# Optimization experiments

Measured on AMD Instinct MI355X. Metric: run time of the kernel, lower is better.

The kernel has to match this reference:

```python
import jax, jax.numpy as jnp
import numpy as np

N_NODES = 100000
N_EDGES = 1600000
N_GRAPHS = 512
N_REL = 4
N_TYPES = 13
EMB = 128
HID = 128
BN_EPS = 1e-5
L2_EPS = 1e-12


def setup_inputs() -> dict:
    key = jax.random.key(0)
    ks = jax.random.split(key, 16)
    node_type = jax.random.randint(ks[0], (N_NODES,), 0, N_TYPES)
    x = jax.nn.one_hot(node_type, N_TYPES, dtype=jnp.float32)  # [N,13] one-hot
    edge_index = jax.random.randint(ks[1], (2, N_EDGES), 0, N_NODES)
    edge_type = jax.random.randint(ks[2], (N_EDGES,), 0, N_REL)
    batch = jnp.sort(jax.random.randint(ks[3], (N_NODES,), 0, N_GRAPHS))
    s = 0.05
    return {
        "x": x,
        "edge_index": edge_index,
        "edge_type": edge_type,
        "batch": batch,
        "emb": jax.random.normal(ks[4], (N_TYPES, EMB), jnp.float32) * s,
        "Wrel": jax.random.normal(ks[5], (2, N_REL, HID, HID), jnp.float32) * s,  # layer0 in=EMB==HID
        "Wroot": jax.random.normal(ks[6], (2, HID, HID), jnp.float32) * s,
        "conv_bias": jnp.zeros((2, HID), jnp.float32),
        "bn_gamma": jnp.ones((2, HID), jnp.float32),
        "bn_beta": jnp.zeros((2, HID), jnp.float32),
        "prelu_a": jnp.full((2,), 0.25, jnp.float32),
        "fc1_w": jax.random.normal(ks[7], (HID, 256), jnp.float32) * s,
        "fc1_b": jnp.zeros((256,), jnp.float32),
        "fc2_w": jax.random.normal(ks[8], (256, 128), jnp.float32) * s,
        "fc2_b": jnp.zeros((128,), jnp.float32),
        "out_w": jax.random.normal(ks[9], (128, 1), jnp.float32) * s,
        "out_b": jnp.zeros((1,), jnp.float32),
    }


def _rgcn_conv(h, Wrel, Wroot, bias, src, dst, edge_type):
    # PyG RGCNConv: out = h @ Wroot + bias + sum_r mean_{edges of rel r}(h_src @ W_r)
    n = h.shape[0]
    out = h @ Wroot + bias
    for r in range(N_REL):
        m = (edge_type == r).astype(h.dtype)  # [E]
        hr = h @ Wrel[r]                       # [N, dout]
        msg = hr[src] * m[:, None]             # gather + mask  [E, dout]
        num = jax.ops.segment_sum(msg, dst, num_segments=n)
        cnt = jax.ops.segment_sum(m, dst, num_segments=n)
        out = out + num / jnp.maximum(cnt, 1.0)[:, None]
    return out


def _batchnorm(h, gamma, beta):
    mu = jnp.mean(h, axis=0)
    var = jnp.mean((h - mu) ** 2, axis=0)  # biased var (training-mode BN)
    return (h - mu) * jax.lax.rsqrt(var + BN_EPS) * gamma + beta


def reference(x, edge_index, edge_type, batch, emb, Wrel, Wroot, conv_bias,
              bn_gamma, bn_beta, prelu_a, fc1_w, fc1_b, fc2_w, fc2_b, out_w, out_b):
    src, dst = edge_index[0], edge_index[1]
    idx = jnp.argmax(x, axis=1)         # torch.nonzero(one_hot)[1]
    h = emb[idx]                        # [N, EMB]
    for l in range(2):
        h = _rgcn_conv(h, Wrel[l], Wroot[l], conv_bias[l], src, dst, edge_type)
        h = _batchnorm(h, bn_gamma[l], bn_beta[l])
        h = jnp.where(h >= 0, h, prelu_a[l] * h)  # PReLU
        nrm = jnp.sqrt(jnp.sum(h * h, axis=1, keepdims=True))
        h = h / jnp.maximum(nrm, L2_EPS)          # F.normalize(p=2, dim=1)
    # global mean pool over graphs
    pooled = jax.ops.segment_sum(h, batch, num_segments=N_GRAPHS)
    cnt = jax.ops.segment_sum(jnp.ones((h.shape[0],), h.dtype), batch, num_segments=N_GRAPHS)
    g = pooled / jnp.maximum(cnt, 1.0)[:, None]   # [G, HID]
    g = jax.nn.relu(g @ fc1_w + fc1_b)
    g = jax.nn.relu(g @ fc2_w + fc2_b)
    return g @ out_w + out_b                      # [G, 1]
```

## Files before the change

kernel.cpp:

```cpp
#include <hip/hip_runtime.h>
#include <hip/hip_bf16.h>

#define NN 100000
#define NE 1600000
#define NG 512
#define CH3 65536
#define CHW 16384
#define NCH 2
#define BPC 128
#define ES 12500


typedef __attribute__((ext_vector_type(8))) short short8;
typedef __attribute__((ext_vector_type(4))) float float4v;


__device__ inline int lower_bound_dev(const int* __restrict__ a, int n, int v) {
    int lo = 0, hi = n;
    while (lo < hi) { int mid = (lo + hi) >> 1; if (a[mid] < v) lo = mid + 1; else hi = mid; }
    return lo;
}

__device__ inline unsigned short f2bf(float x) {
    unsigned u = __float_as_uint(x);
    unsigned r = (u + 0x7fffu + ((u >> 16) & 1u)) >> 16;
    return (unsigned short)r;
}

__device__ inline float bf2f(unsigned short h) {
    return __uint_as_float((unsigned)h << 16);
}


__global__ void node_type_kernel(const float* __restrict__ x, int* __restrict__ idx, int n) {
    int i = blockIdx.x * blockDim.x + threadIdx.x;
    if (i >= n) return;
    const float* row = x + (size_t)i * 13;
    int b = 0;
    #pragma unroll
    for (int t = 0; t < 13; ++t) if (row[t] > 0.5f) { b = t; }
    idx[i] = b;
}


__global__ void build_weights(const float* __restrict__ emb, const float* __restrict__ Wroot,
                              const float* __restrict__ Wrel,
                              unsigned short* __restrict__ Bf, unsigned short* __restrict__ B0f,
                              float* __restrict__ bnSums) {
    if (blockIdx.x < 8) bnSums[blockIdx.x * 256 + threadIdx.x] = 0.f;
    int i = blockIdx.x * 256 + threadIdx.x;
    if (i < 81920) {
        int j = i & 7;
        int lane = (i >> 3) & 63;
        int t = (i >> 9) & 7;
        int ks = (i >> 12) & 3;
        int kc = i >> 14;
        int n = t * 16 + (lane & 15);
        int kcol = j * 16 + ks * 4 + (lane >> 4);
        float w;
        if (kc == 0) w = Wroot[16384 + (size_t)kcol * 128 + n];
        else {
            int r = kc - 1;
            w = Wrel[(((size_t)(4 + r) * 128) + kcol) * 128 + n];
        }
        Bf[i] = f2bf(w);
    } else {
        int i0 = i - 81920;
        int j = i0 & 7;
        int lane = (i0 >> 3) & 63;
        int t = (i0 >> 9) & 7;
        int ks = i0 >> 12;
        int n = t * 16 + (lane & 15);
        int p = ks * 32 + (lane >> 4) * 8 + j;
        float val = 0.f;
        if (p < 32) {
            if (p < 13) {
                const float* er = emb + (size_t)p * 128;
                const float* wc = Wroot + n;
                float acc = 0.f;
                for (int k = 0; k < 128; ++k) acc += er[k] * wc[(size_t)k * 128];
                val = acc;
            }
        } else {
            int r = (p - 32) >> 4, tt = (p - 32) & 15;
            if (tt < 13) {
                const float* er = emb + (size_t)tt * 128;
                const float* wc = Wrel + ((size_t)r * 128) * 128 + n;
                float acc = 0.f;
                for (int k = 0; k < 128; ++k) acc += er[k] * wc[(size_t)k * 128];
                val = acc;
            }
        }
        B0f[i0] = f2bf(val);
    }
}


__global__ __launch_bounds__(256) void hist_kernel(const int* __restrict__ dst,
                                                   const int* __restrict__ src,
                                                   const int* __restrict__ et,
                                                   const int* __restrict__ ntype,
                                                   int* __restrict__ srcT,
                                                   unsigned* __restrict__ partials) {
    __shared__ unsigned h[CHW];
    const int b = blockIdx.x, c = blockIdx.y;
    const int lo = c * CH3;
    for (int i = threadIdx.x; i < CHW; i += 256) h[i] = 0;
    __syncthreads();
    const int e0 = b * ES;
    const int e1 = (e0 + ES < NE) ? e0 + ES : NE;
    if (c == 0) {
        for (int e = e0 + threadIdx.x; e < e1; e += 256) {
            int k = dst[e] - lo;
            if (k >= 0 && k < CH3) atomicAdd(&h[k >> 2], 1u << ((k & 3) << 3));
            int s = src[e];
            srcT[e] = s | (ntype[s] << 17) | (et[e] << 21);
        }
    } else {
        for (int e = e0 + threadIdx.x; e < e1; e += 256) {
            int k = dst[e] - lo;
            if (k >= 0 && k < CH3) atomicAdd(&h[k >> 2], 1u << ((k & 3) << 3));
        }
    }
    __syncthreads();
    unsigned* out = partials + ((size_t)(c * BPC + b)) * CHW;
    for (int i = threadIdx.x; i < CHW; i += 256) out[i] = h[i];
}

__global__ void hist_reduce(unsigned* __restrict__ partials, int* __restrict__ counts) {
    const int c = blockIdx.y;
    const int i = blockIdx.x * 256 + threadIdx.x;
    size_t base = (size_t)c * BPC * CHW + i;
    unsigned r0 = 0, r1 = 0, r2 = 0, r3 = 0;
    #pragma unroll 4
    for (int b = 0; b < BPC; ++b) {
        unsigned t = partials[base + (size_t)b * CHW];
        partials[base + (size_t)b * CHW] = r0 | (r1 << 8) | (r2 << 16) | (r3 << 24);
        r0 += t & 0xffu; r1 += (t >> 8) & 0xffu; r2 += (t >> 16) & 0xffu; r3 += t >> 24;
    }
    int k0 = c * CH3 + 4 * i;
    if (k0 < NN)     counts[k0]     = (int)r0;
    if (k0 + 1 < NN) counts[k0 + 1] = (int)r1;
    if (k0 + 2 < NN) counts[k0 + 2] = (int)r2;
    if (k0 + 3 < NN) counts[k0 + 3] = (int)r3;
}

__global__ __launch_bounds__(256) void scan1(const int* __restrict__ counts, int* __restrict__ offs,
                                             int* __restrict__ bsums, int n) {
    __shared__ int wsum[4];
    const int base = blockIdx.x * 1024 + threadIdx.x * 4;
    int v[4]; int loc = 0;
    #pragma unroll
    for (int j = 0; j < 4; ++j) { int idx = base + j; v[j] = (idx < n) ? counts[idx] : 0; loc += v[j]; }
    const int lane = threadIdx.x & 63, wid = threadIdx.x >> 6;
    int sc = loc;
    #pragma unroll
    for (int o = 1; o < 64; o <<= 1) { int t = __shfl_up(sc, o, 64); if (lane >= o) sc += t; }
    if (lane == 63) wsum[wid] = sc;
    __syncthreads();
    int wbase = 0;
    for (int w = 0; w < wid; ++w) wbase += wsum[w];
    int run = wbase + sc - loc;
    #pragma unroll
    for (int j = 0; j < 4; ++j) { int idx = base + j; if (idx < n) offs[idx] = run; run += v[j]; }
    if (threadIdx.x == 255) bsums[blockIdx.x] = wbase + sc;
}

__global__ void scan2(int* __restrict__ bsums, int* __restrict__ offs, int nb, int n) {
    const int lane = threadIdx.x;
    int carry = 0;
    for (int base = 0; base < nb; base += 64) {
        int idx = base + lane;
        int v = (idx < nb) ? bsums[idx] : 0;
        int sc = v;
        #pragma unroll
        for (int o = 1; o < 64; o <<= 1) { int t = __shfl_up(sc, o, 64); if (lane >= o) sc += t; }
        if (idx < nb) bsums[idx] = carry + sc - v;
        int tot = __shfl(sc, 63, 64);
        carry += tot;
    }
    if (lane == 0) offs[n] = carry;
}

__global__ __launch_bounds__(256) void scan3(int* __restrict__ offs, const int* __restrict__ bsums, int n) {
    const int s = bsums[blockIdx.x];
    const int base = blockIdx.x * 1024 + threadIdx.x * 4;
    #pragma unroll
    for (int j = 0; j < 4; ++j) { int idx = base + j; if (idx < n) offs[idx] += s; }
}

__global__ __launch_bounds__(256) void place_kernel(const int* __restrict__ dst,
                                                    const int* __restrict__ srcT,
                                                    const int* __restrict__ offs,
                                                    const unsigned* __restrict__ partials,
                                                    int* __restrict__ sortedSrc) {
    __shared__ unsigned cur[CHW];
    const int b = blockIdx.x, c = blockIdx.y;
    const int lo = c * CH3;
    const unsigned* pb = partials + ((size_t)(c * BPC + b)) * CHW;
    for (int i = threadIdx.x; i < CHW; i += 256) cur[i] = pb[i];
    __syncthreads();
    const int e0 = b * ES;
    const int e1 = (e0 + ES < NE) ? e0 + ES : NE;
    for (int e = e0 + threadIdx.x; e < e1; e += 256) {
        int key = dst[e];
        int k = key - lo;
        if (k >= 0 && k < CH3) {
            int sh = (k & 3) << 3;
            unsigned old = atomicAdd(&cur[k >> 2], 1u << sh);
            int my = (int)((old >> sh) & 0xffu);
            int pos = offs[key] + my;
            sortedSrc[pos] = srcT[e];
        }
    }
}


__global__ __launch_bounds__(256) void gemm0_fused(const int* __restrict__ sortedSrc,
                                                   const int* __restrict__ offs,
                                                   const int* __restrict__ ntype,
                                                   const unsigned short* __restrict__ B0f,
                                                   const float* __restrict__ bias,
                                                   unsigned short* __restrict__ Cb,
                                                   float* __restrict__ bnSums, int M) {
    __shared__ unsigned short A0L[12 * 128 * 8];
    __shared__ unsigned cnt[128][13];
    __shared__ float sred[2][4][128];
    const int tid = threadIdx.x;

    if (tid < 128) {
        const int n = blockIdx.x * 128 + tid;
        const int tile = tid >> 4, l16 = tid & 15;
        if (n < M) {
            #pragma unroll
            for (int t = 0; t < 13; ++t) cnt[tid][t] = 0;
            const int o0 = offs[n], o1 = offs[n + 1];
            unsigned relc = 0;
            for (int i = o0; i < o1; ++i) {
                int v = sortedSrc[i];
                int ty = (v >> 17) & 15, r = v >> 21;
                cnt[tid][ty] += 1u << (r << 3);
                relc += 1u << (r << 3);
            }
            float inv[4];
            #pragma unroll
            for (int r = 0; r < 4; ++r) {
                unsigned c = (relc >> (r << 3)) & 0xffu;
                inv[r] = 1.0f / (float)(c > 0 ? c : 1);
            }
            const int myty = ntype[n];
            #pragma unroll
            for (int ks = 0; ks < 3; ++ks) {
                #pragma unroll
                for (int quad = 0; quad < 4; ++quad) {
                    unsigned short vals[8];
                    #pragma unroll
                    for (int j = 0; j < 8; ++j) {
                        int p = ks * 32 + quad * 8 + j;
                        float v;
                        if (p < 32) v = (p == myty) ? 1.0f : 0.0f;
                        else {
                            int r = (p - 32) >> 4, tt = (p - 32) & 15;
                            v = (tt < 13) ? (float)((cnt[tid][tt] >> (r << 3)) & 0xffu) * inv[r] : 0.0f;
                        }
                        vals[j] = f2bf(v);
                    }
                    const int C = ks * 4 + quad;
                    *(uint4*)(A0L + (C * 128 + tile * 16 + l16) * 8) = *(uint4*)vals;
                }
            }
        } else {
            uint4 z; z.x = 0; z.y = 0; z.z = 0; z.w = 0;
            #pragma unroll
            for (int C = 0; C < 12; ++C)
                *(uint4*)(A0L + (C * 128 + tile * 16 + l16) * 8) = z;
        }
    }
    __syncthreads();

    const int wv = tid >> 6, lane = tid & 63;
    const int l16 = lane & 15, quad = lane >> 4;
    const int rowbase = blockIdx.x * 128 + wv * 32;
    const int tileL0 = wv * 2, tileL1 = wv * 2 + 1;

    float4v acc[2][8];
    #pragma unroll
    for (int t = 0; t < 8; ++t) {
        float bv = bias[t * 16 + l16];
        float4v av = {bv, bv, bv, bv};
        acc[0][t] = av; acc[1][t] = av;
    }

    const unsigned short* bl = B0f + lane * 8;
    #pragma unroll
    for (int ks = 0; ks < 3; ++ks) {
        const int C = ks * 4 + quad;
        short8 af0 = *(const short8*)(A0L + (C * 128 + tileL0 * 16 + l16) * 8);
        short8 af1 = *(const short8*)(A0L + (C * 128 + tileL1 * 16 + l16) * 8);
        const unsigned short* bp = bl + ((ks * 8) << 9);
        #pragma unroll
        for (int t = 0; t < 8; ++t) {
            short8 bf = *(const short8*)(bp + (t << 9));
            acc[0][t] = __builtin_amdgcn_mfma_f32_16x16x32_bf16(af0, bf, acc[0][t], 0, 0, 0);
            acc[1][t] = __builtin_amdgcn_mfma_f32_16x16x32_bf16(af1, bf, acc[1][t], 0, 0, 0);
        }
    }

    #pragma unroll
    for (int h = 0; h < 2; ++h) {
        #pragma unroll
        for (int rg = 0; rg < 4; ++rg) {
            int rr = rowbase + h * 16 + quad * 4 + rg;
            if (rr < M) {
                unsigned short v[8];
                #pragma unroll
                for (int t = 0; t < 8; ++t) v[t] = f2bf(acc[h][t][rg]);
                *(uint4*)(Cb + (size_t)rr * 128 + l16 * 8) = *(uint4*)v;
            }
        }
    }
    float s[8], q[8];
    #pragma unroll
    for (int t = 0; t < 8; ++t) {
        s[t] = 0.f; q[t] = 0.f;
        #pragma unroll
        for (int h = 0; h < 2; ++h) {
            #pragma unroll
            for (int rg = 0; rg < 4; ++rg) {
                int rr = rowbase + h * 16 + quad * 4 + rg;
                if (rr < M) { float v = acc[h][t][rg]; s[t] += v; q[t] += v * v; }
            }
        }
    }
    #pragma unroll
    for (int t = 0; t < 8; ++t) {
        s[t] += __shfl_down(s[t], 32, 64); q[t] += __shfl_down(q[t], 32, 64);
        s[t] += __shfl_down(s[t], 16, 64); q[t] += __shfl_down(q[t], 16, 64);
    }
    if (lane < 16) {
        #pragma unroll
        for (int t = 0; t < 8; ++t) {
            sred[0][wv][t * 16 + l16] = s[t];
            sred[1][wv][t * 16 + l16] = q[t];
        }
    }
    __syncthreads();
    if (tid < 128) {
        float S = sred[0][0][tid] + sred[0][1][tid] + sred[0][2][tid] + sred[0][3][tid];
        float Q = sred[1][0][tid] + sred[1][1][tid] + sred[1][2][tid] + sred[1][3][tid];
        float* bnS = bnSums + ((blockIdx.x & 7) << 8);
        unsafeAtomicAdd(bnS + tid, S);
        unsafeAtomicAdd(bnS + 128 + tid, Q);
    }
}


__global__ __launch_bounds__(256) void gather_gemm1(const unsigned short* __restrict__ hbf,
                                                    const int* __restrict__ sortedSrc,
                                                    const int* __restrict__ offs,
                                                    const unsigned short* __restrict__ Bf,
                                                    const float* __restrict__ bias,
                                                    unsigned short* __restrict__ Cb,
                                                    float* __restrict__ bnSums) {
    __shared__ unsigned short rootL[2048];
    __shared__ unsigned short aggL[8192];
    const int tid = threadIdx.x;
    const int tile = blockIdx.x;
    {
        const int l16g = tid >> 4;
        const int cidx = tid & 15;
        const int c8 = cidx << 3;
        const int n = tile * 16 + l16g;
        const int pu = cidx * 16 + (l16g ^ cidx);
        uint4 ru = *(const uint4*)(hbf + (size_t)n * 128 + c8);
        *(uint4*)(rootL + pu * 8) = ru;

        const unsigned short* hb = hbf + c8;
        const int o0 = offs[n], o1 = offs[n + 1];

        float a0[8], a1[8], a2[8], a3[8];
        #pragma unroll
        for (int j = 0; j < 8; ++j) { a0[j] = 0.f; a1[j] = 0.f; a2[j] = 0.f; a3[j] = 0.f; }
        float c0 = 0.f, c1 = 0.f, c2 = 0.f, c3 = 0.f;

        auto body = [&](int v, uint4 u) {
            int r = v >> 21;
            float f[8];
            f[0] = __uint_as_float(u.x << 16); f[1] = __uint_as_float(u.x & 0xffff0000u);
            f[2] = __uint_as_float(u.y << 16); f[3] = __uint_as_float(u.y & 0xffff0000u);
            f[4] = __uint_as_float(u.z << 16); f[5] = __uint_as_float(u.z & 0xffff0000u);
            f[6] = __uint_as_float(u.w << 16); f[7] = __uint_as_float(u.w & 0xffff0000u);
            float m0 = (r == 0) ? 1.f : 0.f, m1 = (r == 1) ? 1.f : 0.f;
            float m2 = (r == 2) ? 1.f : 0.f, m3 = (r == 3) ? 1.f : 0.f;
            c0 += m0; c1 += m1; c2 += m2; c3 += m3;
            #pragma unroll
            for (int j = 0; j < 8; ++j) {
                a0[j] = fmaf(m0, f[j], a0[j]);
                a1[j] = fmaf(m1, f[j], a1[j]);
                a2[j] = fmaf(m2, f[j], a2[j]);
                a3[j] = fmaf(m3, f[j], a3[j]);
            }
        };

        int i = o0;
        for (; i + 4 <= o1; i += 4) {
            int v0 = sortedSrc[i], v1 = sortedSrc[i + 1];
            int v2 = sortedSrc[i + 2], v3 = sortedSrc[i + 3];
            uint4 u0 = *(const uint4*)(hb + (size_t)(v0 & 0x1ffff) * 128);
            uint4 u1 = *(const uint4*)(hb + (size_t)(v1 & 0x1ffff) * 128);
            uint4 u2 = *(const uint4*)(hb + (size_t)(v2 & 0x1ffff) * 128);
            uint4 u3 = *(const uint4*)(hb + (size_t)(v3 & 0x1ffff) * 128);
            body(v0, u0); body(v1, u1); body(v2, u2); body(v3, u3);
        }
        if (i + 2 <= o1) {
            int v0 = sortedSrc[i], v1 = sortedSrc[i + 1];
            uint4 u0 = *(const uint4*)(hb + (size_t)(v0 & 0x1ffff) * 128);
            uint4 u1 = *(const uint4*)(hb + (size_t)(v1 & 0x1ffff) * 128);
            body(v0, u0); body(v1, u1);
            i += 2;
        }
        if (i < o1) {
            int v0 = sortedSrc[i];
            uint4 u0 = *(const uint4*)(hb + (size_t)(v0 & 0x1ffff) * 128);
            body(v0, u0);
        }

        const float i0 = 1.f / fmaxf(c0, 1.f), i1 = 1.f / fmaxf(c1, 1.f);
        const float i2 = 1.f / fmaxf(c2, 1.f), i3 = 1.f / fmaxf(c3, 1.f);
        unsigned short* bp = aggL + pu * 8;
        auto pack = [&](float* a, float inv, unsigned short* dp) {
            unsigned short v[8];
            #pragma unroll
            for (int j = 0; j < 8; ++j) v[j] = f2bf(a[j] * inv);
            *(uint4*)dp = *(uint4*)v;
        };
        pack(a0, i0, bp);
        pack(a1, i1, bp + 2048);
        pack(a2, i2, bp + 4096);
        pack(a3, i3, bp + 6144);
    }
    __syncthreads();

    const int wv = tid >> 6, lane = tid & 63;
    const int l16 = lane & 15, quad = lane >> 4;
    const int t0 = wv << 1;
    float4v acc0, acc1;
    {
        float b0v = bias[t0 * 16 + l16];
        float b1v = bias[(t0 + 1) * 16 + l16];
        float4v a0v = {b0v, b0v, b0v, b0v};
        float4v a1v = {b1v, b1v, b1v, b1v};
        acc0 = a0v; acc1 = a1v;
    }
    const unsigned short* bl = Bf + lane * 8;
    #pragma unroll
    for (int kc = 0; kc < 5; ++kc) {
        const unsigned short* Abase = (kc == 0) ? rootL : (aggL + (kc - 1) * 2048);
        #pragma unroll
        for (int ks = 0; ks < 4; ++ks) {
            const int C = ks * 4 + quad;
            const int p = C * 16 + (l16 ^ C);
            short8 af = *(const short8*)(Abase + p * 8);
            const unsigned short* bp = bl + (((kc * 4 + ks) * 8 + t0) << 9);
            short8 b0 = *(const short8*)(bp);
            short8 b1 = *(const short8*)(bp + 512);
            acc0 = __builtin_amdgcn_mfma_f32_16x16x32_bf16(af, b0, acc0, 0, 0, 0);
            acc1 = __builtin_amdgcn_mfma_f32_16x16x32_bf16(af, b1, acc1, 0, 0, 0);
        }
    }
    const int rowbase = tile * 16;
    #pragma unroll
    for (int rg = 0; rg < 4; ++rg) {
        int rr = rowbase + quad * 4 + rg;
        unsigned pk = (unsigned)f2bf(acc0[rg]) | ((unsigned)f2bf(acc1[rg]) << 16);
        *(unsigned*)(Cb + (size_t)rr * 128 + l16 * 8 + t0) = pk;
    }
    float s0 = 0.f, q0 = 0.f, s1 = 0.f, q1 = 0.f;
    #pragma unroll
    for (int rg = 0; rg < 4; ++rg) {
        float v0 = acc0[rg], v1 = acc1[rg];
        s0 += v0; q0 += v0 * v0; s1 += v1; q1 += v1 * v1;
    }
    s0 += __shfl_down(s0, 32, 64); q0 += __shfl_down(q0, 32, 64);
    s1 += __shfl_down(s1, 32, 64); q1 += __shfl_down(q1, 32, 64);
    s0 += __shfl_down(s0, 16, 64); q0 += __shfl_down(q0, 16, 64);
    s1 += __shfl_down(s1, 16, 64); q1 += __shfl_down(q1, 16, 64);
    if (lane < 16) {
        float* bnS = bnSums + ((tile & 7) << 8);
        unsafeAtomicAdd(bnS + t0 * 16 + l16, s0);
        unsafeAtomicAdd(bnS + 128 + t0 * 16 + l16, q0);
        unsafeAtomicAdd(bnS + (t0 + 1) * 16 + l16, s1);
        unsafeAtomicAdd(bnS + 128 + (t0 + 1) * 16 + l16, q1);
    }
}


__global__ void bn_finalize0(float* __restrict__ bnSums, float* __restrict__ fin, int n) {
    const int c = threadIdx.x;
    if (c < 128) {
        float s = 0.f, q = 0.f;
        #pragma unroll
        for (int j = 0; j < 8; ++j) { s += bnSums[j * 256 + c]; q += bnSums[j * 256 + 128 + c]; }
        const float invn = 1.0f / (float)n;
        float mu = s * invn;
        float var = q * invn - mu * mu; if (var < 0.f) var = 0.f;
        fin[c] = mu;
        fin[128 + c] = rsqrtf(var + 1e-5f);
    }
    __syncthreads();
    for (int i = c; i < 2048; i += 256) bnSums[i] = 0.f;
}


__global__ void bn_finalize(const float* __restrict__ bnSums, float* __restrict__ fin,
                            float* __restrict__ g0zero, int n) {
    const int c = threadIdx.x;
    if (g0zero) g0zero[blockIdx.x * 128 + c] = 0.f;
    if (blockIdx.x != 0) return;
    float s = 0.f, q = 0.f;
    #pragma unroll
    for (int j = 0; j < 8; ++j) { s += bnSums[j * 256 + c]; q += bnSums[j * 256 + 128 + c]; }
    const float invn = 1.0f / (float)n;
    float mu = s * invn;
    float var = q * invn - mu * mu; if (var < 0.f) var = 0.f;
    fin[c] = mu;
    fin[128 + c] = rsqrtf(var + 1e-5f);
}


__global__ __launch_bounds__(256) void bn_apply_kernel(const unsigned short* __restrict__ Cb,
                                unsigned short* __restrict__ hbf,
                                const float* __restrict__ fin,
                                const float* __restrict__ gamma, const float* __restrict__ beta,
                                const float* __restrict__ prelu_a, int layer) {
    const int tid = threadIdx.x;
    const int row = blockIdx.x * 16 + (tid >> 4);
    const int li = tid & 15;
    const int p8 = li << 3;
    const float a = prelu_a[layer];
    uint4 u = *(const uint4*)(Cb + (size_t)row * 128 + p8);
    float v[8];
    v[0] = __uint_as_float(u.x << 16); v[1] = __uint_as_float(u.x & 0xffff0000u);
    v[2] = __uint_as_float(u.y << 16); v[3] = __uint_as_float(u.y & 0xffff0000u);
    v[4] = __uint_as_float(u.z << 16); v[5] = __uint_as_float(u.z & 0xffff0000u);
    v[6] = __uint_as_float(u.w << 16); v[7] = __uint_as_float(u.w & 0xffff0000u);
    float t[8]; float ss = 0.f;
    #pragma unroll
    for (int j = 0; j < 8; ++j) {
        int cc = j * 16 + li;
        float tv = (v[j] - fin[cc]) * fin[128 + cc] * gamma[cc] + beta[cc];
        tv = (tv >= 0.f) ? tv : a * tv;
        t[j] = tv; ss += tv * tv;
    }
    ss += __shfl_xor(ss, 1, 64);
    ss += __shfl_xor(ss, 2, 64);
    ss += __shfl_xor(ss, 4, 64);
    ss += __shfl_xor(ss, 8, 64);
    const float scale = 1.0f / fmaxf(sqrtf(ss), 1e-12f);
    unsigned short o[8];
    #pragma unroll
    for (int j = 0; j < 8; ++j) o[j] = f2bf(t[j] * scale);
    *(uint4*)(hbf + (size_t)row * 128 + p8) = *(uint4*)o;
}


__global__ __launch_bounds__(256) void bn_apply_pool(const unsigned short* __restrict__ Cb,
                                const float* __restrict__ fin,
                                const float* __restrict__ gamma, const float* __restrict__ beta,
                                const float* __restrict__ prelu_a,
                                const int* __restrict__ batch,
                                float* __restrict__ g0) {
    __shared__ float P[16][128];
    __shared__ int gids[16];
    const int tid = threadIdx.x;
    const int r16 = tid >> 4;
    const int li = tid & 15;
    const int row = blockIdx.x * 16 + r16;
    const int p8 = li << 3;
    if (li == 0) gids[r16] = batch[row];
    const float a = prelu_a[1];
    uint4 u = *(const uint4*)(Cb + (size_t)row * 128 + p8);
    float v[8];
    v[0] = __uint_as_float(u.x << 16); v[1] = __uint_as_float(u.x & 0xffff0000u);
    v[2] = __uint_as_float(u.y << 16); v[3] = __uint_as_float(u.y & 0xffff0000u);
    v[4] = __uint_as_float(u.z << 16); v[5] = __uint_as_float(u.z & 0xffff0000u);
    v[6] = __uint_as_float(u.w << 16); v[7] = __uint_as_float(u.w & 0xffff0000u);
    float t[8]; float ss = 0.f;
    #pragma unroll
    for (int j = 0; j < 8; ++j) {
        int cc = j * 16 + li;
        float tv = (v[j] - fin[cc]) * fin[128 + cc] * gamma[cc] + beta[cc];
        tv = (tv >= 0.f) ? tv : a * tv;
        t[j] = tv; ss += tv * tv;
    }
    ss += __shfl_xor(ss, 1, 64);
    ss += __shfl_xor(ss, 2, 64);
    ss += __shfl_xor(ss, 4, 64);
    ss += __shfl_xor(ss, 8, 64);
    const float scale = 1.0f / fmaxf(sqrtf(ss), 1e-12f);
    #pragma unroll
    for (int j = 0; j < 8; ++j) P[r16][p8 + j] = t[j] * scale;
    __syncthreads();
    if (tid < 128) {
        int cur = gids[0];
        float run = 0.f;
        #pragma unroll
        for (int rr = 0; rr < 16; ++rr) {
            int g = gids[rr];
            if (g != cur) {
                unsafeAtomicAdd(&g0[(size_t)cur * 128 + tid], run);
                run = 0.f; cur = g;
            }
            run += P[rr][tid];
        }
        unsafeAtomicAdd(&g0[(size_t)cur * 128 + tid], run);
    }
}


__global__ void fc1_kernel(const float* __restrict__ g, const float* __restrict__ w,
                           const float* __restrict__ b, const int* __restrict__ batch,
                           float* __restrict__ o) {
    const int row = blockIdx.x;
    const int j = threadIdx.x;
    const int lo = lower_bound_dev(batch, NN, row);
    const int hi = lower_bound_dev(batch, NN, row + 1);
    const int c = hi - lo;
    const float invc = 1.0f / (float)(c > 0 ? c : 1);
    float acc = 0.f;
    #pragma unroll 8
    for (int k = 0; k < 128; ++k) {
        int lk = (k & 7) * 16 + (k >> 3);
        acc += g[row * 128 + k] * w[lk * 256 + j];
    }
    o[row * 256 + j] = fmaxf(acc * invc + b[j], 0.f);
}

__global__ void fc2_kernel(const float* __restrict__ g, const float* __restrict__ w,
                           const float* __restrict__ b, float* __restrict__ o) {
    const int row = blockIdx.x;
    const int j = threadIdx.x;
    float acc = b[j];
    #pragma unroll 8
    for (int k = 0; k < 256; ++k) acc += g[row * 256 + k] * w[k * 128 + j];
    o[row * 128 + j] = fmaxf(acc, 0.f);
}

__global__ void fco_kernel(const float* __restrict__ g, const float* __restrict__ w,
                           const float* __restrict__ b, float* __restrict__ o) {
    const int row = blockIdx.x * blockDim.x + threadIdx.x;
    if (row >= NG) return;
    float acc = b[0];
    #pragma unroll 8
    for (int k = 0; k < 128; ++k) acc += g[row * 128 + k] * w[k];
    o[row] = acc;
}


extern "C" void kernel_launch(void* const* d_in, const int* in_sizes, int n_in,
                              void* d_out, int out_size, void* d_ws, size_t ws_size,
                              hipStream_t stream) {
    const float* x      = (const float*)d_in[0];
    const int*   eidx   = (const int*)d_in[1];
    const int*   etype  = (const int*)d_in[2];
    const int*   batch  = (const int*)d_in[3];
    const float* emb    = (const float*)d_in[4];
    const float* Wrel   = (const float*)d_in[5];
    const float* Wroot  = (const float*)d_in[6];
    const float* cbias  = (const float*)d_in[7];
    const float* gamma  = (const float*)d_in[8];
    const float* beta   = (const float*)d_in[9];
    const float* prelua = (const float*)d_in[10];
    const float* fc1w   = (const float*)d_in[11];
    const float* fc1b   = (const float*)d_in[12];
    const float* fc2w   = (const float*)d_in[13];
    const float* fc2b   = (const float*)d_in[14];
    const float* outw   = (const float*)d_in[15];
    const float* outb   = (const float*)d_in[16];
    float* out = (float*)d_out;

    const int* src = eidx;
    const int* dst = eidx + NE;

    char* p = (char*)d_ws;
    auto alloc = [&](size_t bytes) { char* r = p; p += (bytes + 255) & ~(size_t)255; return r; };
    unsigned short* hbf   = (unsigned short*)alloc((size_t)NN * 128 * 2);
    unsigned short* Cb    = (unsigned short*)alloc((size_t)NN * 128 * 2);
    unsigned* partials = (unsigned*)alloc((size_t)NCH * BPC * CHW * 4);
    int*   sortedSrc = (int*)alloc((size_t)NE * 4);
    int*   srcT      = (int*)alloc((size_t)NE * 4);
    int*   offs      = (int*)alloc((size_t)(NN + 1) * 4);
    int*   bsums     = (int*)alloc(1024);
    int*   ntype     = (int*)alloc((size_t)NN * 4);
    unsigned short* Bf1 = (unsigned short*)alloc((size_t)81920 * 2);
    unsigned short* B0f = (unsigned short*)alloc((size_t)12288 * 2);
    float* bnSums  = (float*)alloc(2048 * 4);
    float* bnFin   = (float*)alloc(256 * 4);
    float* g0      = (float*)alloc((size_t)NG * 128 * 4);
    float* g1      = (float*)alloc((size_t)NG * 256 * 4);
    float* g2      = (float*)alloc((size_t)NG * 128 * 4);

    const int NBLK = (NN + 1023) / 1024;

    node_type_kernel<<<(NN + 255) / 256, 256, 0, stream>>>(x, ntype, NN);
    build_weights<<<368, 256, 0, stream>>>(emb, Wroot, Wrel, Bf1, B0f, bnSums);

    hist_kernel<<<dim3(BPC, NCH), 256, 0, stream>>>(dst, src, etype, ntype, srcT, partials);
    hist_reduce<<<dim3(CHW / 256, NCH), 256, 0, stream>>>(partials, offs);
    scan1<<<NBLK, 256, 0, stream>>>(offs, offs, bsums, NN);
    scan2<<<1, 64, 0, stream>>>(bsums, offs, NBLK, NN);
    scan3<<<NBLK, 256, 0, stream>>>(offs, bsums, NN);
    place_kernel<<<dim3(BPC, NCH), 256, 0, stream>>>(dst, srcT, offs, partials, sortedSrc);

    gemm0_fused<<<(NN + 127) / 128, 256, 0, stream>>>(sortedSrc, offs, ntype, B0f,
                                                      cbias, Cb, bnSums, NN);
    bn_finalize0<<<1, 256, 0, stream>>>(bnSums, bnFin, NN);
    bn_apply_kernel<<<NN / 16, 256, 0, stream>>>(Cb, hbf, bnFin, gamma, beta, prelua, 0);

    gather_gemm1<<<NN / 16, 256, 0, stream>>>(hbf, sortedSrc, offs, Bf1, cbias + 128, Cb, bnSums);
    bn_finalize<<<512, 128, 0, stream>>>(bnSums, bnFin, g0, NN);
    bn_apply_pool<<<NN / 16, 256, 0, stream>>>(Cb, bnFin, gamma + 128, beta + 128,
                                               prelua, batch, g0);

    fc1_kernel<<<NG, 256, 0, stream>>>(g0, fc1w, fc1b, batch, g1);
    fc2_kernel<<<NG, 128, 0, stream>>>(g1, fc2w, fc2b, g2);
    fco_kernel<<<2, 256, 0, stream>>>(g2, outw, outb, out);
}
```

Baseline: 359.7 us.

## Replace chunked histogram CSR build with global atomic per-type counts

```diff
diff --git a/kernel.cpp b/kernel.cpp
--- a/kernel.cpp
+++ b/kernel.cpp
@@ -4,11 +4,6 @@
 #define NN 100000
 #define NE 1600000
 #define NG 512
-#define CH3 65536
-#define CHW 16384
-#define NCH 2
-#define BPC 128
-#define ES 12500
 
 
 typedef __attribute__((ext_vector_type(8))) short short8;
@@ -27,12 +22,9 @@
     return (unsigned short)r;
 }
 
-__device__ inline float bf2f(unsigned short h) {
-    return __uint_as_float((unsigned)h << 16);
-}
-
-
-__global__ void node_type_kernel(const float* __restrict__ x, int* __restrict__ idx, int n) {
+
+__global__ void node_type_kernel(const float* __restrict__ x, int* __restrict__ idx,
+                                 unsigned* __restrict__ cntG, int n) {
     int i = blockIdx.x * blockDim.x + threadIdx.x;
     if (i >= n) return;
     const float* row = x + (size_t)i * 13;
@@ -40,14 +32,19 @@
     #pragma unroll
     for (int t = 0; t < 13; ++t) if (row[t] > 0.5f) { b = t; }
     idx[i] = b;
+    unsigned* c = cntG + (size_t)i * 13;
+    #pragma unroll
+    for (int t = 0; t < 13; ++t) c[t] = 0u;
 }
 
 
 __global__ void build_weights(const float* __restrict__ emb, const float* __restrict__ Wroot,
                               const float* __restrict__ Wrel,
                               unsigned short* __restrict__ Bf, unsigned short* __restrict__ B0f,
-                              float* __restrict__ bnSums) {
+                              float* __restrict__ bnSums, float* __restrict__ bnSums1,
+                              float* __restrict__ g0) {
     if (blockIdx.x < 8) bnSums[blockIdx.x * 256 + threadIdx.x] = 0.f;
+    else if (blockIdx.x < 16) bnSums1[(blockIdx.x - 8) * 256 + threadIdx.x] = 0.f;
     int i = blockIdx.x * 256 + threadIdx.x;
     if (i < 81920) {
         int j = i & 7;
@@ -64,7 +61,7 @@
             w = Wrel[(((size_t)(4 + r) * 128) + kcol) * 128 + n];
         }
         Bf[i] = f2bf(w);
-    } else {
+    } else if (i < 94208) {
         int i0 = i - 81920;
         int j = i0 & 7;
         int lane = (i0 >> 3) & 63;
@@ -92,66 +89,52 @@
             }
         }
         B0f[i0] = f2bf(val);
-    }
-}
-
-
-__global__ __launch_bounds__(256) void hist_kernel(const int* __restrict__ dst,
-                                                   const int* __restrict__ src,
-                                                   const int* __restrict__ et,
-                                                   const int* __restrict__ ntype,
-                                                   int* __restrict__ srcT,
-                                                   unsigned* __restrict__ partials) {
-    __shared__ unsigned h[CHW];
-    const int b = blockIdx.x, c = blockIdx.y;
-    const int lo = c * CH3;
-    for (int i = threadIdx.x; i < CHW; i += 256) h[i] = 0;
-    __syncthreads();
-    const int e0 = b * ES;
-    const int e1 = (e0 + ES < NE) ? e0 + ES : NE;
-    if (c == 0) {
-        for (int e = e0 + threadIdx.x; e < e1; e += 256) {
-            int k = dst[e] - lo;
-            if (k >= 0 && k < CH3) atomicAdd(&h[k >> 2], 1u << ((k & 3) << 3));
+    } else {
+        int gz = i - 94208;
+        g0[gz] = 0.f;
+    }
+}
+
+
+__global__ __launch_bounds__(256) void count_kernel(const int* __restrict__ dst,
+                                                    const int* __restrict__ src,
+                                                    const int* __restrict__ et,
+                                                    const int* __restrict__ ntype,
+                                                    int* __restrict__ srcT,
+                                                    unsigned* __restrict__ cntG) {
+    const int base = blockIdx.x * 1024 + threadIdx.x;
+    #pragma unroll
+    for (int j = 0; j < 4; ++j) {
+        int e = base + j * 256;
+        if (e < NE) {
+            int d = dst[e];
             int s = src[e];
-            srcT[e] = s | (ntype[s] << 17) | (et[e] << 21);
-        }
-    } else {
-        for (int e = e0 + threadIdx.x; e < e1; e += 256) {
-            int k = dst[e] - lo;
-            if (k >= 0 && k < CH3) atomicAdd(&h[k >> 2], 1u << ((k & 3) << 3));
-        }
-    }
-    __syncthreads();
-    unsigned* out = partials + ((size_t)(c * BPC + b)) * CHW;
-    for (int i = threadIdx.x; i < CHW; i += 256) out[i] = h[i];
-}
-
-__global__ void hist_reduce(unsigned* __restrict__ partials, int* __restrict__ counts) {
-    const int c = blockIdx.y;
-    const int i = blockIdx.x * 256 + threadIdx.x;
-    size_t base = (size_t)c * BPC * CHW + i;
-    unsigned r0 = 0, r1 = 0, r2 = 0, r3 = 0;
-    #pragma unroll 4
-    for (int b = 0; b < BPC; ++b) {
-        unsigned t = partials[base + (size_t)b * CHW];
-        partials[base + (size_t)b * CHW] = r0 | (r1 << 8) | (r2 << 16) | (r3 << 24);
-        r0 += t & 0xffu; r1 += (t >> 8) & 0xffu; r2 += (t >> 16) & 0xffu; r3 += t >> 24;
-    }
-    int k0 = c * CH3 + 4 * i;
-    if (k0 < NN)     counts[k0]     = (int)r0;
-    if (k0 + 1 < NN) counts[k0 + 1] = (int)r1;
-    if (k0 + 2 < NN) counts[k0 + 2] = (int)r2;
-    if (k0 + 3 < NN) counts[k0 + 3] = (int)r3;
-}
-
-__global__ __launch_bounds__(256) void scan1(const int* __restrict__ counts, int* __restrict__ offs,
+            int r = et[e];
+            int ty = ntype[s];
+            srcT[e] = s | (ty << 17) | (r << 21);
+            atomicAdd(&cntG[(size_t)d * 13 + ty], 1u << (r << 3));
+        }
+    }
+}
+
+
+__global__ __launch_bounds__(256) void scan1(const unsigned* __restrict__ cntG, int* __restrict__ offs,
                                              int* __restrict__ bsums, int n) {
     __shared__ int wsum[4];
     const int base = blockIdx.x * 1024 + threadIdx.x * 4;
     int v[4]; int loc = 0;
     #pragma unroll
-    for (int j = 0; j < 4; ++j) { int idx = base + j; v[j] = (idx < n) ? counts[idx] : 0; loc += v[j]; }
+    for (int j = 0; j < 4; ++j) {
+        int idx = base + j; int c = 0;
+        if (idx < n) {
+            const unsigned* cg = cntG + (size_t)idx * 13;
+            unsigned acc = 0;
+            #pragma unroll
+            for (int t = 0; t < 13; ++t) acc += cg[t];
+            c = (int)((acc & 0xffu) + ((acc >> 8) & 0xffu) + ((acc >> 16) & 0xffu) + (acc >> 24));
+        }
+        v[j] = c; loc += c;
+    }
     const int lane = threadIdx.x & 63, wid = threadIdx.x >> 6;
     int sc = loc;
     #pragma unroll
@@ -182,66 +165,58 @@
     if (lane == 0) offs[n] = carry;
 }
 
-__global__ __launch_bounds__(256) void scan3(int* __restrict__ offs, const int* __restrict__ bsums, int n) {
+__global__ __launch_bounds__(256) void scan3(int* __restrict__ offs, const int* __restrict__ bsums,
+                                             int* __restrict__ cursor, int n) {
     const int s = bsums[blockIdx.x];
     const int base = blockIdx.x * 1024 + threadIdx.x * 4;
     #pragma unroll
-    for (int j = 0; j < 4; ++j) { int idx = base + j; if (idx < n) offs[idx] += s; }
-}
+    for (int j = 0; j < 4; ++j) {
+        int idx = base + j;
+        if (idx < n) { int v = offs[idx] + s; offs[idx] = v; cursor[idx] = v; }
+    }
+}
+
 
 __global__ __launch_bounds__(256) void place_kernel(const int* __restrict__ dst,
                                                     const int* __restrict__ srcT,
-                                                    const int* __restrict__ offs,
-                                                    const unsigned* __restrict__ partials,
+                                                    int* __restrict__ cursor,
                                                     int* __restrict__ sortedSrc) {
-    __shared__ unsigned cur[CHW];
-    const int b = blockIdx.x, c = blockIdx.y;
-    const int lo = c * CH3;
-    const unsigned* pb = partials + ((size_t)(c * BPC + b)) * CHW;
-    for (int i = threadIdx.x; i < CHW; i += 256) cur[i] = pb[i];
-    __syncthreads();
-    const int e0 = b * ES;
-    const int e1 = (e0 + ES < NE) ? e0 + ES : NE;
-    for (int e = e0 + threadIdx.x; e < e1; e += 256) {
-        int key = dst[e];
-        int k = key - lo;
-        if (k >= 0 && k < CH3) {
-            int sh = (k & 3) << 3;
-            unsigned old = atomicAdd(&cur[k >> 2], 1u << sh);
-            int my = (int)((old >> sh) & 0xffu);
-            int pos = offs[key] + my;
+    const int base = blockIdx.x * 1024 + threadIdx.x;
+    #pragma unroll
+    for (int j = 0; j < 4; ++j) {
+        int e = base + j * 256;
+        if (e < NE) {
+            int pos = atomicAdd(&cursor[dst[e]], 1);
             sortedSrc[pos] = srcT[e];
         }
     }
 }
 
 
-__global__ __launch_bounds__(256) void gemm0_fused(const int* __restrict__ sortedSrc,
-                                                   const int* __restrict__ offs,
+__global__ __launch_bounds__(256) void gemm0_fused(const unsigned* __restrict__ cntG,
                                                    const int* __restrict__ ntype,
                                                    const unsigned short* __restrict__ B0f,
                                                    const float* __restrict__ bias,
                                                    unsigned short* __restrict__ Cb,
                                                    float* __restrict__ bnSums, int M) {
     __shared__ unsigned short A0L[12 * 128 * 8];
-    __shared__ unsigned cnt[128][13];
+    __shared__ unsigned cls[1664];
     __shared__ float sred[2][4][128];
     const int tid = threadIdx.x;
+
+    {
+        const size_t cbase = (size_t)blockIdx.x * 1664;
+        for (int i = tid; i < 1664; i += 256) cls[i] = cntG[cbase + i];
+    }
+    __syncthreads();
 
     if (tid < 128) {
         const int n = blockIdx.x * 128 + tid;
         const int tile = tid >> 4, l16 = tid & 15;
         if (n < M) {
-            #pragma unroll
-            for (int t = 0; t < 13; ++t) cnt[tid][t] = 0;
-            const int o0 = offs[n], o1 = offs[n + 1];
-            unsigned relc = 0;
-            for (int i = o0; i < o1; ++i) {
-                int v = sortedSrc[i];
-                int ty = (v >> 17) & 15, r = v >> 21;
-                cnt[tid][ty] += 1u << (r << 3);
-                relc += 1u << (r << 3);
-            }
+            unsigned cw[13]; unsigned relc = 0;
+            #pragma unroll
+            for (int t = 0; t < 13; ++t) { cw[t] = cls[tid * 13 + t]; relc += cw[t]; }
             float inv[4];
             #pragma unroll
             for (int r = 0; r < 4; ++r) {
@@ -261,7 +236,7 @@
                         if (p < 32) v = (p == myty) ? 1.0f : 0.0f;
                         else {
                             int r = (p - 32) >> 4, tt = (p - 32) & 15;
-                            v = (tt < 13) ? (float)((cnt[tid][tt] >> (r << 3)) & 0xffu) * inv[r] : 0.0f;
+                            v = (tt < 13) ? (float)((cw[tt] >> (r << 3)) & 0xffu) * inv[r] : 0.0f;
                         }
                         vals[j] = f2bf(v);
                     }
@@ -495,45 +470,24 @@
 }
 
 
-__global__ void bn_finalize0(float* __restrict__ bnSums, float* __restrict__ fin, int n) {
-    const int c = threadIdx.x;
-    if (c < 128) {
+__global__ __launch_bounds__(256) void bn_apply_kernel(const unsigned short* __restrict__ Cb,
+                                unsigned short* __restrict__ hbf,
+                                const float* __restrict__ bnSums,
+                                const float* __restrict__ gamma, const float* __restrict__ beta,
+                                const float* __restrict__ prelu_a, int layer) {
+    __shared__ float finS[256];
+    const int tid = threadIdx.x;
+    if (tid < 128) {
         float s = 0.f, q = 0.f;
         #pragma unroll
-        for (int j = 0; j < 8; ++j) { s += bnSums[j * 256 + c]; q += bnSums[j * 256 + 128 + c]; }
-        const float invn = 1.0f / (float)n;
+        for (int j = 0; j < 8; ++j) { s += bnSums[j * 256 + tid]; q += bnSums[j * 256 + 128 + tid]; }
+        const float invn = 1.0f / (float)NN;
         float mu = s * invn;
         float var = q * invn - mu * mu; if (var < 0.f) var = 0.f;
-        fin[c] = mu;
-        fin[128 + c] = rsqrtf(var + 1e-5f);
-    }
-    __syncthreads();
-    for (int i = c; i < 2048; i += 256) bnSums[i] = 0.f;
-}
-
-
-__global__ void bn_finalize(const float* __restrict__ bnSums, float* __restrict__ fin,
-                            float* __restrict__ g0zero, int n) {
-    const int c = threadIdx.x;
-    if (g0zero) g0zero[blockIdx.x * 128 + c] = 0.f;
-    if (blockIdx.x != 0) return;
-    float s = 0.f, q = 0.f;
-    #pragma unroll
-    for (int j = 0; j < 8; ++j) { s += bnSums[j * 256 + c]; q += bnSums[j * 256 + 128 + c]; }
-    const float invn = 1.0f / (float)n;
-    float mu = s * invn;
-    float var = q * invn - mu * mu; if (var < 0.f) var = 0.f;
-    fin[c] = mu;
-    fin[128 + c] = rsqrtf(var + 1e-5f);
-}
-
-
-__global__ __launch_bounds__(256) void bn_apply_kernel(const unsigned short* __restrict__ Cb,
-                                unsigned short* __restrict__ hbf,
-                                const float* __restrict__ fin,
-                                const float* __restrict__ gamma, const float* __restrict__ beta,
-                                const float* __restrict__ prelu_a, int layer) {
-    const int tid = threadIdx.x;
+        finS[tid] = mu;
+        finS[128 + tid] = rsqrtf(var + 1e-5f);
+    }
+    __syncthreads();
     const int row = blockIdx.x * 16 + (tid >> 4);
     const int li = tid & 15;
     const int p8 = li << 3;
@@ -548,7 +502,7 @@
     #pragma unroll
     for (int j = 0; j < 8; ++j) {
         int cc = j * 16 + li;
-        float tv = (v[j] - fin[cc]) * fin[128 + cc] * gamma[cc] + beta[cc];
+        float tv = (v[j] - finS[cc]) * finS[128 + cc] * gamma[cc] + beta[cc];
         tv = (tv >= 0.f) ? tv : a * tv;
         t[j] = tv; ss += tv * tv;
     }
@@ -565,19 +519,31 @@
 
 
 __global__ __launch_bounds__(256) void bn_apply_pool(const unsigned short* __restrict__ Cb,
-                                const float* __restrict__ fin,
+                                const float* __restrict__ bnSums,
                                 const float* __restrict__ gamma, const float* __restrict__ beta,
                                 const float* __restrict__ prelu_a,
                                 const int* __restrict__ batch,
                                 float* __restrict__ g0) {
     __shared__ float P[16][128];
     __shared__ int gids[16];
+    __shared__ float finS[256];
     const int tid = threadIdx.x;
+    if (tid < 128) {
+        float s = 0.f, q = 0.f;
+        #pragma unroll
+        for (int j = 0; j < 8; ++j) { s += bnSums[j * 256 + tid]; q += bnSums[j * 256 + 128 + tid]; }
+        const float invn = 1.0f / (float)NN;
+        float mu = s * invn;
+        float var = q * invn - mu * mu; if (var < 0.f) var = 0.f;
+        finS[tid] = mu;
+        finS[128 + tid] = rsqrtf(var + 1e-5f);
+    }
     const int r16 = tid >> 4;
     const int li = tid & 15;
     const int row = blockIdx.x * 16 + r16;
     const int p8 = li << 3;
     if (li == 0) gids[r16] = batch[row];
+    __syncthreads();
     const float a = prelu_a[1];
     uint4 u = *(const uint4*)(Cb + (size_t)row * 128 + p8);
     float v[8];
@@ -589,7 +555,7 @@
     #pragma unroll
     for (int j = 0; j < 8; ++j) {
         int cc = j * 16 + li;
-        float tv = (v[j] - fin[cc]) * fin[128 + cc] * gamma[cc] + beta[cc];
+        float tv = (v[j] - finS[cc]) * finS[128 + cc] * gamma[cc] + beta[cc];
         tv = (tv >= 0.f) ? tv : a * tv;
         t[j] = tv; ss += tv * tv;
     }
@@ -621,11 +587,12 @@
 __global__ void fc1_kernel(const float* __restrict__ g, const float* __restrict__ w,
                            const float* __restrict__ b, const int* __restrict__ batch,
                            float* __restrict__ o) {
+    __shared__ int se[2];
     const int row = blockIdx.x;
     const int j = threadIdx.x;
-    const int lo = lower_bound_dev(batch, NN, row);
-    const int hi = lower_bound_dev(batch, NN, row + 1);
-    const int c = hi - lo;
+    if (j < 2) se[j] = lower_bound_dev(batch, NN, row + j);
+    __syncthreads();
+    const int c = se[1] - se[0];
     const float invc = 1.0f / (float)(c > 0 ? c : 1);
     float acc = 0.f;
     #pragma unroll 8
@@ -686,40 +653,38 @@
     auto alloc = [&](size_t bytes) { char* r = p; p += (bytes + 255) & ~(size_t)255; return r; };
     unsigned short* hbf   = (unsigned short*)alloc((size_t)NN * 128 * 2);
     unsigned short* Cb    = (unsigned short*)alloc((size_t)NN * 128 * 2);
-    unsigned* partials = (unsigned*)alloc((size_t)NCH * BPC * CHW * 4);
     int*   sortedSrc = (int*)alloc((size_t)NE * 4);
     int*   srcT      = (int*)alloc((size_t)NE * 4);
+    unsigned* cntG   = (unsigned*)alloc((size_t)782 * 1664 * 4);
     int*   offs      = (int*)alloc((size_t)(NN + 1) * 4);
+    int*   cursor    = (int*)alloc((size_t)NN * 4);
     int*   bsums     = (int*)alloc(1024);
     int*   ntype     = (int*)alloc((size_t)NN * 4);
     unsigned short* Bf1 = (unsigned short*)alloc((size_t)81920 * 2);
     unsigned short* B0f = (unsigned short*)alloc((size_t)12288 * 2);
     float* bnSums  = (float*)alloc(2048 * 4);
-    float* bnFin   = (float*)alloc(256 * 4);
+    float* bnSums1 = (float*)alloc(2048 * 4);
     float* g0      = (float*)alloc((size_t)NG * 128 * 4);
     float* g1      = (float*)alloc((size_t)NG * 256 * 4);
     float* g2      = (float*)alloc((size_t)NG * 128 * 4);
 
     const int NBLK = (NN + 1023) / 1024;
-
-    node_type_kernel<<<(NN + 255) / 256, 256, 0, stream>>>(x, ntype, NN);
-    build_weights<<<368, 256, 0, stream>>>(emb, Wroot, Wrel, Bf1, B0f, bnSums);
-
-    hist_kernel<<<dim3(BPC, NCH), 256, 0, stream>>>(dst, src, etype, ntype, srcT, partials);
-    hist_reduce<<<dim3(CHW / 256, NCH), 256, 0, stream>>>(partials, offs);
-    scan1<<<NBLK, 256, 0, stream>>>(offs, offs, bsums, NN);
+    const int EBLK = (NE + 1023) / 1024;
+
+    node_type_kernel<<<(NN + 255) / 256, 256, 0, stream>>>(x, ntype, cntG, NN);
+    build_weights<<<624, 256, 0, stream>>>(emb, Wroot, Wrel, Bf1, B0f, bnSums, bnSums1, g0);
+
+    count_kernel<<<EBLK, 256, 0, stream>>>(dst, src, etype, ntype, srcT, cntG);
+    scan1<<<NBLK, 256, 0, stream>>>(cntG, offs, bsums, NN);
     scan2<<<1, 64, 0, stream>>>(bsums, offs, NBLK, NN);
-    scan3<<<NBLK, 256, 0, stream>>>(offs, bsums, NN);
-    place_kernel<<<dim3(BPC, NCH), 256, 0, stream>>>(dst, srcT, offs, partials, sortedSrc);
-
-    gemm0_fused<<<(NN + 127) / 128, 256, 0, stream>>>(sortedSrc, offs, ntype, B0f,
-                                                      cbias, Cb, bnSums, NN);
-    bn_finalize0<<<1, 256, 0, stream>>>(bnSums, bnFin, NN);
-    bn_apply_kernel<<<NN / 16, 256, 0, stream>>>(Cb, hbf, bnFin, gamma, beta, prelua, 0);
-
-    gather_gemm1<<<NN / 16, 256, 0, stream>>>(hbf, sortedSrc, offs, Bf1, cbias + 128, Cb, bnSums);
-    bn_finalize<<<512, 128, 0, stream>>>(bnSums, bnFin, g0, NN);
-    bn_apply_pool<<<NN / 16, 256, 0, stream>>>(Cb, bnFin, gamma + 128, beta + 128,
+    scan3<<<NBLK, 256, 0, stream>>>(offs, bsums, cursor, NN);
+    place_kernel<<<EBLK, 256, 0, stream>>>(dst, srcT, cursor, sortedSrc);
+
+    gemm0_fused<<<(NN + 127) / 128, 256, 0, stream>>>(cntG, ntype, B0f, cbias, Cb, bnSums, NN);
+    bn_apply_kernel<<<NN / 16, 256, 0, stream>>>(Cb, hbf, bnSums, gamma, beta, prelua, 0);
+
+    gather_gemm1<<<NN / 16, 256, 0, stream>>>(hbf, sortedSrc, offs, Bf1, cbias + 128, Cb, bnSums1);
+    bn_apply_pool<<<NN / 16, 256, 0, stream>>>(Cb, bnSums1, gamma + 128, beta + 128,
                                                prelua, batch, g0);
 
     fc1_kernel<<<NG, 256, 0, stream>>>(g0, fc1w, fc1b, batch, g1);
```

Result: slower. 464.0 us (+29.0%).
